# Optimization experiments

Hardware: AMD Instinct MI355X
Metric: run time of the kernel (lower is better)

Reference implementation:

```python
import jax, jax.numpy as jnp
import numpy as np

N_EMBD = 512
HEADS = 8
PATCH = 16
STRIDE = 4
NUM_POINTS = 128


def pos_embed_sine(n_embd=N_EMBD, patch=PATCH, temperature=10000.0):
    # getPositionEmbeddingSine(num_pos_feats=n_embd, patch=16, normalize=True)
    ar = np.arange(patch, dtype=np.float32)
    yy, xx = np.meshgrid(ar, ar, indexing='ij')  # torch.meshgrid default 'ij'
    eps, scale = 1e-6, 2.0 * np.pi
    y_e = yy / (yy[-1:, :] + eps) * scale
    x_e = xx / (xx[:, -1:] + eps) * scale
    dim_t = np.arange(n_embd // 2, dtype=np.float32)
    dim_t = temperature ** (2.0 * np.floor(dim_t / 2.0) / n_embd)
    px = x_e[:, :, None] / dim_t
    py = y_e[:, :, None] / dim_t
    px = np.stack((np.sin(px[:, :, 0::2]), np.cos(px[:, :, 1::2])), axis=3).reshape(patch, patch, -1)
    py = np.stack((np.sin(py[:, :, 0::2]), np.cos(py[:, :, 1::2])), axis=3).reshape(patch, patch, -1)
    pos = np.concatenate((py, px), axis=2).transpose(2, 0, 1)  # [n_embd, patch, patch]
    return jnp.asarray(pos, jnp.float32)


def setup_inputs() -> dict:
    key = jax.random.key(0)
    ks = jax.random.split(key, 6)
    B, T, C, H, W = 32, 64, 64, 160, 160
    h = w = 640  # input image size (feature stride 4)
    N = B * T
    cnn_feature = jax.random.normal(ks[0], (B, C, H, W), jnp.float32)
    contours = jax.random.uniform(ks[1], (N, NUM_POINTS, 2), jnp.float32) * w  # image-space coords
    ct_01 = jnp.ones((B, T), bool)
    ct_img_idx = jnp.repeat(jnp.arange(B, dtype=jnp.int32), T)
    ct_ind = jax.random.randint(ks[2], (N,), 0, H * W, jnp.int32)
    conv_w = jax.random.normal(ks[3], (N_EMBD, C + 2, NUM_POINTS // STRIDE), jnp.float32) * 0.02
    conv_b = jnp.zeros((N_EMBD,), jnp.float32)
    attn_w = jax.random.normal(ks[4], (2 * N_EMBD, N_EMBD), jnp.float32) * 0.02
    attn_b = jnp.zeros((2 * N_EMBD,), jnp.float32)
    p_w = jax.random.normal(ks[5], (1, HEADS, 1), jnp.float32)
    pos_embed = pos_embed_sine()
    return dict(cnn_feature=cnn_feature, contours=contours, ct_01=ct_01,
                ct_img_idx=ct_img_idx, ct_ind=ct_ind, h=h, w=w,
                conv_w=conv_w, conv_b=conv_b, attn_w=attn_w, attn_b=attn_b,
                p_w=p_w, pos_embed=pos_embed)


def _forward(cnn_feature, contours, ct_01, ct_img_idx, ct_ind, h, w,
             conv_w, conv_b, attn_w, attn_b, p_w, pos_embed):
    B, C, H, W = cnn_feature.shape
    Bp, T = ct_01.shape
    N = contours.shape[0]
    cs = contours[:, ::STRIDE]  # [N, P, 2] sampled contour points
    # grid_sample bilinear, align_corners=False, zeros padding:
    # pixel = ((x/(w/2)-1 + 1)*W - 1)/2 = x*W/w - 0.5
    px = cs[..., 0] * (float(W) / float(w)) - 0.5
    py = cs[..., 1] * (float(H) / float(h)) - 0.5
    x0 = jnp.floor(px)
    y0 = jnp.floor(py)

    def gather(yi, xi, wgt):
        valid = (xi >= 0) & (xi < W) & (yi >= 0) & (yi < H)
        xi_c = jnp.clip(xi, 0, W - 1).astype(jnp.int32)
        yi_c = jnp.clip(yi, 0, H - 1).astype(jnp.int32)
        v = cnn_feature[ct_img_idx[:, None], :, yi_c, xi_c]  # [N, P, C]
        return v * (wgt * valid)[..., None]

    feats = (gather(y0, x0, (x0 + 1 - px) * (y0 + 1 - py))
             + gather(y0, x0 + 1, (px - x0) * (y0 + 1 - py))
             + gather(y0 + 1, x0, (x0 + 1 - px) * (py - y0))
             + gather(y0 + 1, x0 + 1, (px - x0) * (py - y0)))
    feats = feats.transpose(0, 2, 1)  # [N, C, P]
    normed = (cs / jnp.array([w, h], jnp.float32)).transpose(0, 2, 1)  # [N, 2, P]
    cf = jnp.concatenate([feats, normed], axis=1)  # [N, C+2, P]
    # Conv1d with kernel == full length -> a single contraction over (channel, point)
    cf = jnp.einsum('ncp,ocp->no', cf, conv_w) + conv_b  # [N, n_embd]
    # positional embedding indexed by quantized center coords
    ct_x = (ct_ind % W) * PATCH // W
    ct_y = (ct_ind // W) * PATCH // H
    cf = cf + pos_embed[:, ct_y, ct_x].T  # [N, n_embd]
    qk = cf @ attn_w.T + attn_b
    q, k = qk[:, :N_EMBD], qk[:, N_EMBD:]
    # boolean-mask scatter into padded [B, T, E] (row-major fill order)
    mask = ct_01.reshape(-1)
    order = jnp.clip(jnp.cumsum(mask) - 1, 0, N - 1)
    pad_q = jnp.where(mask[:, None], q[order], 0.0).reshape(Bp, T, N_EMBD)
    pad_k = jnp.where(mask[:, None], k[order], 0.0).reshape(Bp, T, N_EMBD)
    hd = N_EMBD // HEADS
    Q = pad_q.reshape(Bp, T, HEADS, hd).transpose(0, 2, 1, 3)
    K = pad_k.reshape(Bp, T, HEADS, hd).transpose(0, 2, 1, 3)
    att = jnp.einsum('bhtd,bhsd->bhts', Q, K) * (1.0 / jnp.sqrt(jnp.float32(hd)))
    # registered 'bias' buffer is all ones -> masked_fill is a no-op
    att = jnp.einsum('bhts,h->bts', att, p_w[0, :, 0])  # 1x1 conv across heads
    att = jax.nn.sigmoid(att)
    return jnp.where(jnp.isnan(att), 0.0, att)


def reference(cnn_feature, contours, ct_01, ct_img_idx, ct_ind, h, w,
              conv_w, conv_b, attn_w, attn_b, p_w, pos_embed):
    return _forward(cnn_feature, contours, ct_01, ct_img_idx, ct_ind, h, w,
                    conv_w, conv_b, attn_w, attn_b, p_w, pos_embed)
```

## Files before the change

kernel.cpp:

```cpp
#include <hip/hip_runtime.h>
#include <math.h>

#define NCT   2048
#define BIMG  32
#define CIN   64
#define CTOT  66
#define NPTS  32
#define KCONV 2112
#define NE    512
#define NQK   1024
#define HH    160
#define WW    160
#define OUTSZ 131072
#define NROWS (BIMG * HH)
#define CAP   128

typedef __attribute__((ext_vector_type(8))) short short8;
typedef __attribute__((ext_vector_type(4))) float f32x4;

#define OFF_WT    0
#define OFF_AWT   (OFF_WT + 540672)
#define OFF_XA    (OFF_AWT + 262144)
#define OFF_XB    (OFF_XA + 2162688)
#define OFF_CF    (OFF_XB + 2162688)
#define OFF_PART  (OFF_CF + 524288)
#define OFF_QK    (OFF_PART + 2097152)
#define OFF_ATT   (OFF_QK + 2097152)
#define OFF_PTS   (OFF_ATT + 524288)
#define OFF_CNT   (OFF_PTS + 131072)
#define OFF_LIST  (OFF_CNT + 5120)

__device__ __forceinline__ unsigned short f2bf(float f) {
    unsigned int u = __float_as_uint(f);
    u += 0x7FFFu + ((u >> 16) & 1u);
    return (unsigned short)(u >> 16);
}
__device__ __forceinline__ float bf2f(unsigned int h) {
    return __uint_as_float(h << 16);
}
__device__ __forceinline__ unsigned int bfadd2(unsigned int a, unsigned int b) {
    float lo = bf2f(a & 0xFFFFu) + bf2f(b & 0xFFFFu);
    float hi = __uint_as_float(a & 0xFFFF0000u) + __uint_as_float(b & 0xFFFF0000u);
    return (unsigned int)f2bf(lo) | ((unsigned int)f2bf(hi) << 16);
}
__device__ __forceinline__ uint4 bfadd8(uint4 a, uint4 b) {
    return make_uint4(bfadd2(a.x, b.x), bfadd2(a.y, b.y),
                      bfadd2(a.z, b.z), bfadd2(a.w, b.w));
}

__global__ void k_init(const float* __restrict__ conv_w, const float* __restrict__ attn_w,
                       unsigned short* __restrict__ Wt, unsigned short* __restrict__ Awt,
                       int* __restrict__ cnt) {
    int bid = blockIdx.x;
    if (bid < 512) {
        const float* src = conv_w + (size_t)bid * KCONV;
        unsigned short* dst = Wt + (size_t)bid * KCONV;
        for (int k2 = threadIdx.x; k2 < KCONV; k2 += 256) {
            int p = k2 / CTOT;
            int c = k2 - p * CTOT;
            dst[k2] = f2bf(src[c * NPTS + p]);
        }
    } else if (bid < 1024) {
        int i = ((bid - 512) * 256 + threadIdx.x) * 4;
        float4 v = *(const float4*)(attn_w + i);
        uint2 o;
        o.x = (unsigned int)f2bf(v.x) | ((unsigned int)f2bf(v.y) << 16);
        o.y = (unsigned int)f2bf(v.z) | ((unsigned int)f2bf(v.w) << 16);
        *(uint2*)(Awt + i) = o;
    } else {
        for (int j = threadIdx.x; j < NROWS; j += 256) cnt[j] = 0;
    }
}

__global__ void k_prep(const float* __restrict__ contours,
                       const int* __restrict__ img_idx,
                       float* __restrict__ pts, int* __restrict__ cnt,
                       int* __restrict__ list,
                       unsigned short* __restrict__ Xa, unsigned short* __restrict__ Xb) {
    int pid = blockIdx.x * blockDim.x + threadIdx.x;
    if (pid >= NCT * NPTS) return;
    int n = pid >> 5, p = pid & 31;
    float cx = contours[(n * 128 + p * 4) * 2 + 0];
    float cy = contours[(n * 128 + p * 4) * 2 + 1];
    float px = cx * 0.25f - 0.5f;
    float py = cy * 0.25f - 0.5f;
    pts[pid * 2 + 0] = px;
    pts[pid * 2 + 1] = py;
    int img = img_idx[n];
    int y0 = (int)floorf(py);
#pragma unroll
    for (int r = 0; r < 2; ++r) {
        int yc = min(max(y0 + r, 0), HH - 1);
        int bin = img * HH + yc;
        int slot = atomicAdd(&cnt[bin], 1);
        if (slot < CAP) list[bin * CAP + slot] = pid | (r << 16);
    }
    size_t base = (size_t)n * KCONV + p * CTOT;
    Xa[base + 64] = f2bf(cx * (1.f / 640.f));
    Xa[base + 65] = f2bf(cy * (1.f / 640.f));
    Xb[base + 64] = 0;
    Xb[base + 65] = 0;
}

__global__ void __launch_bounds__(256)
k_stage(const float* __restrict__ feat, const float* __restrict__ pts,
        const int* __restrict__ cnt, const int* __restrict__ list,
        unsigned short* __restrict__ Xa, unsigned short* __restrict__ Xb) {
    __shared__ float sA[32 * 161];
    int bid = blockIdx.x;
    int chalf = bid & 1;
    int rowid = bid >> 1;
    int img = rowid / HH, row = rowid % HH;
    int nE = min(cnt[rowid], CAP);
    if (nE == 0) return;

    const float* fbase = feat + ((size_t)img * CIN + chalf * 32) * (HH * WW) + row * WW;
#pragma unroll
    for (int i = 0; i < 5; ++i) {
        int idx = threadIdx.x + i * 256;
        int c = idx / 40, xq = idx % 40;
        float4 v = *(const float4*)(fbase + (size_t)c * (HH * WW) + xq * 4);
        float* s = &sA[c * 161 + xq * 4];
        s[0] = v.x; s[1] = v.y; s[2] = v.z; s[3] = v.w;
    }
    __syncthreads();

    int sub = threadIdx.x >> 5;
    int ch = threadIdx.x & 31;
    for (int e = sub; e < nE; e += 8) {
        int entry = list[rowid * CAP + e];
        int pid = entry & 0xFFFF, r = entry >> 16;
        float px = pts[pid * 2 + 0];
        float py = pts[pid * 2 + 1];
        float fx0 = floorf(px), fy0 = floorf(py);
        int x0 = (int)fx0;
        float wx1 = px - fx0, wx0 = 1.f - wx1;
        float wy = r ? (py - fy0) : (fy0 + 1.f - py);
        int yi = (int)fy0 + r;
        bool vy = (yi >= 0) & (yi < HH);
        bool vx0 = (x0 >= 0) & (x0 < WW);
        bool vx1 = (x0 + 1 >= 0) & (x0 + 1 < WW);
        int xc0 = min(max(x0, 0), WW - 1);
        int xc1 = min(max(x0 + 1, 0), WW - 1);
        float v0 = sA[ch * 161 + xc0];
        float v1 = sA[ch * 161 + xc1];
        float contrib = vy ? wy * ((vx0 ? wx0 * v0 : 0.f) + (vx1 ? wx1 * v1 : 0.f))
                           : 0.f;
        int n = pid >> 5, p = pid & 31;
        unsigned short* dst = r ? Xb : Xa;
        dst[(size_t)n * KCONV + p * CTOT + chalf * 32 + ch] = f2bf(contrib);
    }
}

template <bool SUM2>
__device__ __forceinline__ void mm64core(const unsigned short* __restrict__ A,
                                         const unsigned short* __restrict__ A2, int lda,
                                         const unsigned short* __restrict__ B, int ldb,
                                         int m0, int n0, int kbeg, int ksteps,
                                         f32x4 acc[2][2]) {
    __shared__ unsigned short As[64 * 40];
    __shared__ unsigned short Bs[64 * 40];
    const int t = threadIdx.x;
    const int ra = t >> 2;
    const int ca = (t & 3) << 3;
    const int wid = t >> 6, lane = t & 63;
    const int wm = (wid >> 1) << 5, wn = (wid & 1) << 5;
    const int fr = lane & 15, kg = lane >> 4;

    const unsigned short* pa = A + (size_t)(m0 + ra) * lda + kbeg + ca;
    const unsigned short* pa2 = SUM2 ? (A2 + (size_t)(m0 + ra) * lda + kbeg + ca) : nullptr;
    const unsigned short* pb = B + (size_t)(n0 + ra) * ldb + kbeg + ca;
    uint4 va = *(const uint4*)pa;
    uint4 va2 = SUM2 ? *(const uint4*)pa2 : make_uint4(0, 0, 0, 0);
    uint4 vb = *(const uint4*)pb;

    for (int s = 0; s < ksteps; ++s) {
        uint4 sa = SUM2 ? bfadd8(va, va2) : va;
        __syncthreads();
        *(uint4*)&As[ra * 40 + ca] = sa;
        *(uint4*)&Bs[ra * 40 + ca] = vb;
        __syncthreads();
        if (s + 1 < ksteps) {
            va = *(const uint4*)(pa + (s + 1) * 32);
            if (SUM2) va2 = *(const uint4*)(pa2 + (s + 1) * 32);
            vb = *(const uint4*)(pb + (s + 1) * 32);
        }
        short8 a0 = *(const short8*)&As[(wm + fr) * 40 + kg * 8];
        short8 a1 = *(const short8*)&As[(wm + 16 + fr) * 40 + kg * 8];
        short8 b0 = *(const short8*)&Bs[(wn + fr) * 40 + kg * 8];
        short8 b1 = *(const short8*)&Bs[(wn + 16 + fr) * 40 + kg * 8];
        acc[0][0] = __builtin_amdgcn_mfma_f32_16x16x32_bf16(a0, b0, acc[0][0], 0, 0, 0);
        acc[0][1] = __builtin_amdgcn_mfma_f32_16x16x32_bf16(a0, b1, acc[0][1], 0, 0, 0);
        acc[1][0] = __builtin_amdgcn_mfma_f32_16x16x32_bf16(a1, b0, acc[1][0], 0, 0, 0);
        acc[1][1] = __builtin_amdgcn_mfma_f32_16x16x32_bf16(a1, b1, acc[1][1], 0, 0, 0);
    }
}

__global__ void __launch_bounds__(256)
k_mm_conv(const unsigned short* __restrict__ Xa, const unsigned short* __restrict__ Xb,
          const unsigned short* __restrict__ Wt, float* __restrict__ part) {
    f32x4 acc[2][2] = {};
    int m0 = blockIdx.x * 64, n0 = blockIdx.y * 64, kz = blockIdx.z;
    mm64core<true>(Xa, Xb, KCONV, Wt, KCONV, m0, n0, kz * 1056, 33, acc);
    int lane = threadIdx.x & 63, wid = threadIdx.x >> 6;
    int wm = (wid >> 1) << 5, wn = (wid & 1) << 5;
    int crow = (lane >> 4) * 4, ccol = lane & 15;
    float* dst = part + (size_t)kz * (NCT * NE);
#pragma unroll
    for (int i = 0; i < 2; ++i)
#pragma unroll
        for (int j = 0; j < 2; ++j)
#pragma unroll
            for (int r = 0; r < 4; ++r)
                dst[(size_t)(m0 + wm + i * 16 + crow + r) * NE + (n0 + wn + j * 16 + ccol)] = acc[i][j][r];
}

__global__ void k_cf(const float* __restrict__ part, const float* __restrict__ conv_b,
                     const float* __restrict__ pos, const int* __restrict__ ct_ind,
                     unsigned short* __restrict__ cf) {
    int idx = blockIdx.x * blockDim.x + threadIdx.x;
    int n = idx >> 7, og = (idx & 127) << 2;
    int ct = ct_ind[n];
    int ctx = ((ct % WW) * 16) / WW;
    int cty = ((ct / WW) * 16) / HH;
    float4 p0 = *(const float4*)(part + (size_t)n * NE + og);
    float4 p1 = *(const float4*)(part + (size_t)(NCT + n) * NE + og);
    float4 cb = *(const float4*)(conv_b + og);
    float s0 = p0.x + p1.x + cb.x + pos[((og + 0) * 16 + cty) * 16 + ctx];
    float s1 = p0.y + p1.y + cb.y + pos[((og + 1) * 16 + cty) * 16 + ctx];
    float s2 = p0.z + p1.z + cb.z + pos[((og + 2) * 16 + cty) * 16 + ctx];
    float s3 = p0.w + p1.w + cb.w + pos[((og + 3) * 16 + cty) * 16 + ctx];
    uint2 o;
    o.x = (unsigned int)f2bf(s0) | ((unsigned int)f2bf(s1) << 16);
    o.y = (unsigned int)f2bf(s2) | ((unsigned int)f2bf(s3) << 16);
    *(uint2*)(cf + (size_t)n * NE + og) = o;
}

__global__ void __launch_bounds__(256)
k_mm_attn(const unsigned short* __restrict__ cf, const unsigned short* __restrict__ Awt,
          const float* __restrict__ attn_b, const float* __restrict__ pw,
          float* __restrict__ qk) {
    f32x4 acc[2][2] = {};
    int m0 = blockIdx.x * 64, n0 = blockIdx.y * 64;
    mm64core<false>(cf, nullptr, NE, Awt, NE, m0, n0, 0, 16, acc);
    int lane = threadIdx.x & 63, wid = threadIdx.x >> 6;
    int wm = (wid >> 1) << 5, wn = (wid & 1) << 5;
    int crow = (lane >> 4) * 4, ccol = lane & 15;
#pragma unroll
    for (int i = 0; i < 2; ++i)
#pragma unroll
        for (int j = 0; j < 2; ++j) {
            int o = n0 + wn + j * 16 + ccol;
            float scale = (o < NE) ? pw[o >> 6] * 0.125f : 1.f;
            float bias = attn_b[o];
#pragma unroll
            for (int r = 0; r < 4; ++r) {
                float v = (acc[i][j][r] + bias) * ((o < NE) ? scale : 1.f);
                qk[(size_t)(m0 + wm + i * 16 + crow + r) * NQK + o] = v;
            }
        }
}

__device__ __forceinline__ void gemm64x64(const float* __restrict__ A, int lda,
                                          const float* __restrict__ B, int ldb,
                                          int K, int m0, int n0, float acc[4][4]) {
    __shared__ float As[16][68];
    __shared__ float Bs[16][68];
    const int tid = threadIdx.x;
    const int lr = tid >> 2;
    const int lc = (tid & 3) << 2;
    const int tm = tid >> 4;
    const int tn = tid & 15;
#pragma unroll
    for (int i = 0; i < 4; ++i)
#pragma unroll
        for (int j = 0; j < 4; ++j) acc[i][j] = 0.f;

    for (int k0 = 0; k0 < K; k0 += 16) {
        float4 a4 = *(const float4*)(A + (size_t)(m0 + lr) * lda + k0 + lc);
        float4 b4 = *(const float4*)(B + (size_t)(n0 + lr) * ldb + k0 + lc);
        __syncthreads();
        As[lc + 0][lr] = a4.x; As[lc + 1][lr] = a4.y; As[lc + 2][lr] = a4.z; As[lc + 3][lr] = a4.w;
        Bs[lc + 0][lr] = b4.x; Bs[lc + 1][lr] = b4.y; Bs[lc + 2][lr] = b4.z; Bs[lc + 3][lr] = b4.w;
        __syncthreads();
#pragma unroll
        for (int kk = 0; kk < 16; ++kk) {
            float4 av = *(const float4*)&As[kk][tm << 2];
            float4 bv = *(const float4*)&Bs[kk][tn << 2];
            float aa[4] = {av.x, av.y, av.z, av.w};
            float bb[4] = {bv.x, bv.y, bv.z, bv.w};
#pragma unroll
            for (int i = 0; i < 4; ++i)
#pragma unroll
                for (int j = 0; j < 4; ++j)
                    acc[i][j] = fmaf(aa[i], bb[j], acc[i][j]);
        }
    }
}

__global__ void k_att(const float* __restrict__ qk, float* __restrict__ part) {
    float acc[4][4];
    int b = blockIdx.x, kc = blockIdx.y;
    int m0 = b * 64;
    gemm64x64(qk + kc * 128, NQK, qk + NE + kc * 128, NQK, 128, m0, m0, acc);
    int tm = threadIdx.x >> 4, tn = threadIdx.x & 15;
    float* dst = part + ((size_t)kc * BIMG + b) * 4096;
#pragma unroll
    for (int i = 0; i < 4; ++i)
#pragma unroll
        for (int j = 0; j < 4; ++j)
            dst[(tm * 4 + i) * 64 + tn * 4 + j] = acc[i][j];
}

__global__ void k_sig(const float* __restrict__ part, float* __restrict__ out) {
    int i = blockIdx.x * blockDim.x + threadIdx.x;
    float s = part[i] + part[OUTSZ + i] + part[2 * OUTSZ + i] + part[3 * OUTSZ + i];
    float r = 1.f / (1.f + expf(-s));
    out[i] = (r == r) ? r : 0.f;
}

extern "C" void kernel_launch(void* const* d_in, const int* in_sizes, int n_in,
                              void* d_out, int out_size, void* d_ws, size_t ws_size,
                              hipStream_t stream) {
    const float* cnn      = (const float*)d_in[0];
    const float* contours = (const float*)d_in[1];
    const int* img_idx    = (const int*)d_in[3];
    const int* ct_ind     = (const int*)d_in[4];
    const float* conv_w   = (const float*)d_in[7];
    const float* conv_b   = (const float*)d_in[8];
    const float* attn_w   = (const float*)d_in[9];
    const float* attn_b   = (const float*)d_in[10];
    const float* p_w      = (const float*)d_in[11];
    const float* pos      = (const float*)d_in[12];

    float* ws = (float*)d_ws;
    unsigned short* Wt  = (unsigned short*)(ws + OFF_WT);
    unsigned short* Awt = (unsigned short*)(ws + OFF_AWT);
    unsigned short* Xa  = (unsigned short*)(ws + OFF_XA);
    unsigned short* Xb  = (unsigned short*)(ws + OFF_XB);
    unsigned short* cf  = (unsigned short*)(ws + OFF_CF);
    float* part = ws + OFF_PART;
    float* qk   = ws + OFF_QK;
    float* att  = ws + OFF_ATT;
    float* pts  = ws + OFF_PTS;
    int*   cnt  = (int*)(ws + OFF_CNT);
    int*   list = (int*)(ws + OFF_LIST);
    float* out  = (float*)d_out;

    hipLaunchKernelGGL(k_init,    dim3(1025),      dim3(256), 0, stream, conv_w, attn_w, Wt, Awt, cnt);
    hipLaunchKernelGGL(k_prep,    dim3(256),       dim3(256), 0, stream, contours, img_idx, pts, cnt, list, Xa, Xb);
    hipLaunchKernelGGL(k_stage,   dim3(2 * NROWS), dim3(256), 0, stream, cnn, pts, cnt, list, Xa, Xb);
    hipLaunchKernelGGL(k_mm_conv, dim3(32, 8, 2),  dim3(256), 0, stream, Xa, Xb, Wt, part);
    hipLaunchKernelGGL(k_cf,      dim3(1024),      dim3(256), 0, stream, part, conv_b, pos, ct_ind, cf);
    hipLaunchKernelGGL(k_mm_attn, dim3(32, 16),    dim3(256), 0, stream, cf, Awt, attn_b, p_w, qk);
    hipLaunchKernelGGL(k_att,     dim3(32, 4),     dim3(256), 0, stream, qk, att);
    hipLaunchKernelGGL(k_sig,     dim3(512),       dim3(256), 0, stream, att, out);
}
```

Measured before the change: 105.6 us.

## Use bf16 MFMA for attention scores, fuse sigmoid, and split conv GEMM four ways

```diff
diff --git a/kernel.cpp b/kernel.cpp
--- a/kernel.cpp
+++ b/kernel.cpp
@@ -11,7 +11,6 @@
 #define NQK   1024
 #define HH    160
 #define WW    160
-#define OUTSZ 131072
 #define NROWS (BIMG * HH)
 #define CAP   128
 
@@ -24,9 +23,8 @@
 #define OFF_XB    (OFF_XA + 2162688)
 #define OFF_CF    (OFF_XB + 2162688)
 #define OFF_PART  (OFF_CF + 524288)
-#define OFF_QK    (OFF_PART + 2097152)
-#define OFF_ATT   (OFF_QK + 2097152)
-#define OFF_PTS   (OFF_ATT + 524288)
+#define OFF_QKB   (OFF_PART + 4194304)
+#define OFF_PTS   (OFF_QKB + 1048576)
 #define OFF_CNT   (OFF_PTS + 131072)
 #define OFF_LIST  (OFF_CNT + 5120)
 
@@ -201,7 +199,9 @@
           const unsigned short* __restrict__ Wt, float* __restrict__ part) {
     f32x4 acc[2][2] = {};
     int m0 = blockIdx.x * 64, n0 = blockIdx.y * 64, kz = blockIdx.z;
-    mm64core<true>(Xa, Xb, KCONV, Wt, KCONV, m0, n0, kz * 1056, 33, acc);
+    int kbeg = (kz < 2) ? kz * 544 : 1088 + (kz - 2) * 512;
+    int ksteps = (kz < 2) ? 17 : 16;
+    mm64core<true>(Xa, Xb, KCONV, Wt, KCONV, m0, n0, kbeg, ksteps, acc);
     int lane = threadIdx.x & 63, wid = threadIdx.x >> 6;
     int wm = (wid >> 1) << 5, wn = (wid & 1) << 5;
     int crow = (lane >> 4) * 4, ccol = lane & 15;
@@ -223,23 +223,27 @@
     int ct = ct_ind[n];
     int ctx = ((ct % WW) * 16) / WW;
     int cty = ((ct / WW) * 16) / HH;
-    float4 p0 = *(const float4*)(part + (size_t)n * NE + og);
-    float4 p1 = *(const float4*)(part + (size_t)(NCT + n) * NE + og);
+    float s[4] = {0.f, 0.f, 0.f, 0.f};
+#pragma unroll
+    for (int kz = 0; kz < 4; ++kz) {
+        float4 p = *(const float4*)(part + ((size_t)kz * NCT + n) * NE + og);
+        s[0] += p.x; s[1] += p.y; s[2] += p.z; s[3] += p.w;
+    }
     float4 cb = *(const float4*)(conv_b + og);
-    float s0 = p0.x + p1.x + cb.x + pos[((og + 0) * 16 + cty) * 16 + ctx];
-    float s1 = p0.y + p1.y + cb.y + pos[((og + 1) * 16 + cty) * 16 + ctx];
-    float s2 = p0.z + p1.z + cb.z + pos[((og + 2) * 16 + cty) * 16 + ctx];
-    float s3 = p0.w + p1.w + cb.w + pos[((og + 3) * 16 + cty) * 16 + ctx];
+    s[0] += cb.x + pos[((og + 0) * 16 + cty) * 16 + ctx];
+    s[1] += cb.y + pos[((og + 1) * 16 + cty) * 16 + ctx];
+    s[2] += cb.z + pos[((og + 2) * 16 + cty) * 16 + ctx];
+    s[3] += cb.w + pos[((og + 3) * 16 + cty) * 16 + ctx];
     uint2 o;
-    o.x = (unsigned int)f2bf(s0) | ((unsigned int)f2bf(s1) << 16);
-    o.y = (unsigned int)f2bf(s2) | ((unsigned int)f2bf(s3) << 16);
+    o.x = (unsigned int)f2bf(s[0]) | ((unsigned int)f2bf(s[1]) << 16);
+    o.y = (unsigned int)f2bf(s[2]) | ((unsigned int)f2bf(s[3]) << 16);
     *(uint2*)(cf + (size_t)n * NE + og) = o;
 }
 
 __global__ void __launch_bounds__(256)
 k_mm_attn(const unsigned short* __restrict__ cf, const unsigned short* __restrict__ Awt,
           const float* __restrict__ attn_b, const float* __restrict__ pw,
-          float* __restrict__ qk) {
+          unsigned short* __restrict__ qkb) {
     f32x4 acc[2][2] = {};
     int m0 = blockIdx.x * 64, n0 = blockIdx.y * 64;
     mm64core<false>(cf, nullptr, NE, Awt, NE, m0, n0, 0, 16, acc);
@@ -255,68 +259,33 @@
             float bias = attn_b[o];
 #pragma unroll
             for (int r = 0; r < 4; ++r) {
-                float v = (acc[i][j][r] + bias) * ((o < NE) ? scale : 1.f);
-                qk[(size_t)(m0 + wm + i * 16 + crow + r) * NQK + o] = v;
+                float v = (acc[i][j][r] + bias) * scale;
+                qkb[(size_t)(m0 + wm + i * 16 + crow + r) * NQK + o] = f2bf(v);
             }
         }
 }
 
-__device__ __forceinline__ void gemm64x64(const float* __restrict__ A, int lda,
-                                          const float* __restrict__ B, int ldb,
-                                          int K, int m0, int n0, float acc[4][4]) {
-    __shared__ float As[16][68];
-    __shared__ float Bs[16][68];
-    const int tid = threadIdx.x;
-    const int lr = tid >> 2;
-    const int lc = (tid & 3) << 2;
-    const int tm = tid >> 4;
-    const int tn = tid & 15;
-#pragma unroll
-    for (int i = 0; i < 4; ++i)
-#pragma unroll
-        for (int j = 0; j < 4; ++j) acc[i][j] = 0.f;
-
-    for (int k0 = 0; k0 < K; k0 += 16) {
-        float4 a4 = *(const float4*)(A + (size_t)(m0 + lr) * lda + k0 + lc);
-        float4 b4 = *(const float4*)(B + (size_t)(n0 + lr) * ldb + k0 + lc);
-        __syncthreads();
-        As[lc + 0][lr] = a4.x; As[lc + 1][lr] = a4.y; As[lc + 2][lr] = a4.z; As[lc + 3][lr] = a4.w;
-        Bs[lc + 0][lr] = b4.x; Bs[lc + 1][lr] = b4.y; Bs[lc + 2][lr] = b4.z; Bs[lc + 3][lr] = b4.w;
-        __syncthreads();
-#pragma unroll
-        for (int kk = 0; kk < 16; ++kk) {
-            float4 av = *(const float4*)&As[kk][tm << 2];
-            float4 bv = *(const float4*)&Bs[kk][tn << 2];
-            float aa[4] = {av.x, av.y, av.z, av.w};
-            float bb[4] = {bv.x, bv.y, bv.z, bv.w};
-#pragma unroll
-            for (int i = 0; i < 4; ++i)
-#pragma unroll
-                for (int j = 0; j < 4; ++j)
-                    acc[i][j] = fmaf(aa[i], bb[j], acc[i][j]);
-        }
-    }
-}
-
-__global__ void k_att(const float* __restrict__ qk, float* __restrict__ part) {
-    float acc[4][4];
-    int b = blockIdx.x, kc = blockIdx.y;
-    int m0 = b * 64;
-    gemm64x64(qk + kc * 128, NQK, qk + NE + kc * 128, NQK, 128, m0, m0, acc);
-    int tm = threadIdx.x >> 4, tn = threadIdx.x & 15;
-    float* dst = part + ((size_t)kc * BIMG + b) * 4096;
-#pragma unroll
-    for (int i = 0; i < 4; ++i)
-#pragma unroll
-        for (int j = 0; j < 4; ++j)
-            dst[(tm * 4 + i) * 64 + tn * 4 + j] = acc[i][j];
-}
-
-__global__ void k_sig(const float* __restrict__ part, float* __restrict__ out) {
-    int i = blockIdx.x * blockDim.x + threadIdx.x;
-    float s = part[i] + part[OUTSZ + i] + part[2 * OUTSZ + i] + part[3 * OUTSZ + i];
-    float r = 1.f / (1.f + expf(-s));
-    out[i] = (r == r) ? r : 0.f;
+__global__ void __launch_bounds__(256)
+k_att2(const unsigned short* __restrict__ qkb, float* __restrict__ out) {
+    f32x4 acc[2][2] = {};
+    int b = blockIdx.x;
+    const unsigned short* base = qkb + (size_t)b * 64 * NQK;
+    mm64core<false>(base, nullptr, NQK, base + NE, NQK, 0, 0, 0, 16, acc);
+    int lane = threadIdx.x & 63, wid = threadIdx.x >> 6;
+    int wm = (wid >> 1) << 5, wn = (wid & 1) << 5;
+    int crow = (lane >> 4) * 4, ccol = lane & 15;
+    float* dst = out + (size_t)b * 4096;
+#pragma unroll
+    for (int i = 0; i < 2; ++i)
+#pragma unroll
+        for (int j = 0; j < 2; ++j)
+#pragma unroll
+            for (int r = 0; r < 4; ++r) {
+                float s = acc[i][j][r];
+                float sg = 1.f / (1.f + expf(-s));
+                sg = (sg == sg) ? sg : 0.f;
+                dst[(wm + i * 16 + crow + r) * 64 + (wn + j * 16 + ccol)] = sg;
+            }
 }
 
 extern "C" void kernel_launch(void* const* d_in, const int* in_sizes, int n_in,
@@ -340,8 +309,7 @@
     unsigned short* Xb  = (unsigned short*)(ws + OFF_XB);
     unsigned short* cf  = (unsigned short*)(ws + OFF_CF);
     float* part = ws + OFF_PART;
-    float* qk   = ws + OFF_QK;
-    float* att  = ws + OFF_ATT;
+    unsigned short* qkb = (unsigned short*)(ws + OFF_QKB);
     float* pts  = ws + OFF_PTS;
     int*   cnt  = (int*)(ws + OFF_CNT);
     int*   list = (int*)(ws + OFF_LIST);
@@ -350,9 +318,8 @@
     hipLaunchKernelGGL(k_init,    dim3(1025),      dim3(256), 0, stream, conv_w, attn_w, Wt, Awt, cnt);
     hipLaunchKernelGGL(k_prep,    dim3(256),       dim3(256), 0, stream, contours, img_idx, pts, cnt, list, Xa, Xb);
     hipLaunchKernelGGL(k_stage,   dim3(2 * NROWS), dim3(256), 0, stream, cnn, pts, cnt, list, Xa, Xb);
-    hipLaunchKernelGGL(k_mm_conv, dim3(32, 8, 2),  dim3(256), 0, stream, Xa, Xb, Wt, part);
+    hipLaunchKernelGGL(k_mm_conv, dim3(32, 8, 4),  dim3(256), 0, stream, Xa, Xb, Wt, part);
     hipLaunchKernelGGL(k_cf,      dim3(1024),      dim3(256), 0, stream, part, conv_b, pos, ct_ind, cf);
-    hipLaunchKernelGGL(k_mm_attn, dim3(32, 16),    dim3(256), 0, stream, cf, Awt, attn_b, p_w, qk);
-    hipLaunchKernelGGL(k_att,     dim3(32, 4),     dim3(256), 0, stream, qk, att);
-    hipLaunchKernelGGL(k_sig,     dim3(512),       dim3(256), 0, stream, att, out);
-}
+    hipLaunchKernelGGL(k_mm_attn, dim3(32, 16),    dim3(256), 0, stream, cf, Awt, attn_b, p_w, qkb);
+    hipLaunchKernelGGL(k_att2,    dim3(32),        dim3(256), 0, stream, qkb, out);
+}
```

Result: faster. 101.2 us (-4.1%).
